# Kernel optimization log

Hardware: AMD Instinct MI355X
Metric: run time of the kernel (lower is better)

Reference implementation:

```python
import jax, jax.numpy as jnp
import numpy as np

L, B, T, TC, T1, D, DK, FF = 4, 4, 1024, 1024, 2048, 384, 256, 1536
TT = 0.1   # lamed blending coefficient (tt in (0,1] path)
EPS = 1e-5


def _ln(x, g, b):
    m = jnp.mean(x, axis=-1, keepdims=True)
    v = jnp.mean((x - m) ** 2, axis=-1, keepdims=True)
    return (x - m) * jax.lax.rsqrt(v + EPS) * g + b


def setup_inputs() -> dict:
    key = jax.random.key(0)
    ks = jax.random.split(key, 16)
    s = 0.02
    return {
        "tgt": jax.random.normal(ks[0], (B, T, D), jnp.float32),
        "memory": jax.random.normal(ks[1], (B, T1, DK), jnp.float32),
        "score_c": jax.random.normal(ks[2], (L, B, TC, T1), jnp.float32),
        "out_c": jax.random.normal(ks[3], (L, B, TC, D), jnp.float32),
        "Wq": jax.random.normal(ks[4], (L, D, D), jnp.float32) * s,
        "bq": jnp.zeros((L, D), jnp.float32),
        "Wk": jax.random.normal(ks[5], (L, D, DK), jnp.float32) * s,
        "bk": jnp.zeros((L, D), jnp.float32),
        "Wv": jax.random.normal(ks[6], (L, D, DK), jnp.float32) * s,
        "bv": jnp.zeros((L, D), jnp.float32),
        "Wkn": jax.random.normal(ks[7], (L, D, D), jnp.float32) * s,
        "bkn": jnp.zeros((L, D), jnp.float32),
        "Wun": jax.random.normal(ks[8], (L, D, D), jnp.float32) * s,
        "bun": jnp.zeros((L, D), jnp.float32),
        "W1": jax.random.normal(ks[9], (L, FF, D), jnp.float32) * s,
        "b1": jnp.zeros((L, FF), jnp.float32),
        "W2": jax.random.normal(ks[10], (L, D, FF), jnp.float32) * s,
        "b2": jnp.zeros((L, D), jnp.float32),
        "g1": jnp.ones((L, D), jnp.float32),
        "be1": jnp.zeros((L, D), jnp.float32),
        "g2": jnp.ones((L, D), jnp.float32),
        "be2": jnp.zeros((L, D), jnp.float32),
    }


def reference(tgt, memory, score_c, out_c, Wq, bq, Wk, bk, Wv, bv,
              Wkn, bkn, Wun, bun, W1, b1, W2, b2, g1, be1, g2, be2):
    scale = 1.0 / np.sqrt(D)
    x = tgt
    for l in range(L):  # fixed small layer count
        # cross-attention q/k/v (n_head = 1)
        q = jnp.einsum('btd,ed->bte', x, Wq[l]) + bq[l]            # [B,T,D]
        k = jnp.einsum('bsk,ek->bse', memory, Wk[l]) + bk[l]       # [B,T1,D]
        v = jnp.einsum('bsk,ek->bse', memory, Wv[l]) + bv[l]       # [B,T1,D]
        att = jnp.einsum('bte,bse->bts', q, k) * scale             # [B,T,T1]
        # blended score path (tt in (0,1])
        unk = jnp.einsum('btd,ed->bte', x, Wun[l]) + bun[l]        # [B,T,D]
        kno = jnp.einsum('bcd,ed->bce', out_c[l], Wkn[l]) + bkn[l] # [B,TC,D]
        score1 = jnp.einsum('bte,bce->btc', unk, kno) * scale      # [B,T,TC]
        mixed = jnp.einsum('btc,bcs->bts', score1, score_c[l])     # [B,T,T1]
        blended = TT * jax.nn.softmax(mixed, axis=-1) \
                  + (1.0 - TT) * jax.nn.softmax(att, axis=-1)
        z = jnp.einsum('bts,bse->bte', blended, v)                 # [B,T,D]
        x = _ln(x + z, g1[l], be1[l])
        h = jax.nn.relu(jnp.einsum('btd,fd->btf', x, W1[l]) + b1[l])
        y2 = jnp.einsum('btf,df->btd', h, W2[l]) + b2[l]
        x = _ln(x + y2, g2[l], be2[l])
    return x
```

## Files before the change

### kernel.cpp

```cpp
#include <hip/hip_runtime.h>
#include <math.h>

#define Lc 4
#define Bc 4
#define Tc 1024
#define TCc 1024
#define T1c 2048
#define Dc 384
#define DKc 256
#define FFc 1536
#define TTc 0.1f
#define EPSc 1e-5f

typedef unsigned short u16;
typedef __attribute__((ext_vector_type(8))) __bf16 bf16x8;
typedef __attribute__((ext_vector_type(8))) _Float16 f16x8;
typedef __attribute__((ext_vector_type(4))) float f32x4;

__device__ inline u16 f2bf(float f) {
  union { float f; unsigned u; } x; x.f = f;
  unsigned r = x.u + 0x7fffu + ((x.u >> 16) & 1u);
  return (u16)(r >> 16);
}

struct CDesc { const float* src; u16* dst; long n4; };
struct CPack { CDesc d[16]; long tot4; int nd; };

__global__ void cvt_multi(CPack P) {
  long i = (long)blockIdx.x * 256 + threadIdx.x;
  const long st = (long)gridDim.x * 256;
  for (; i < P.tot4; i += st) {
    long r = i; int g = 0;
    while (g < P.nd - 1 && r >= P.d[g].n4) { r -= P.d[g].n4; ++g; }
    float4 v = ((const float4*)P.d[g].src)[r];
    ushort4 o;
    o.x = f2bf(v.x); o.y = f2bf(v.y); o.z = f2bf(v.z); o.w = f2bf(v.w);
    ((ushort4*)P.d[g].dst)[r] = o;
  }
}

__global__ void concat_bias(const float* __restrict__ a, const float* __restrict__ b,
                            float* __restrict__ o) {
  int l = blockIdx.x, t = threadIdx.x;
  o[l * 768 + t] = (t < Dc) ? a[l * Dc + t] : b[l * Dc + t - Dc];
}

__global__ __launch_bounds__(256) void transpose_cvt(const float* __restrict__ src,
                                                     u16* __restrict__ dst) {
  __shared__ float t[64 * 65];
  const int z = blockIdx.z;
  const float* s = src + (long)z * TCc * T1c;
  u16* d = dst + (long)z * T1c * TCc;
  const int s0 = blockIdx.x * 64, c0 = blockIdx.y * 64;
  const int tc = threadIdx.x >> 4;
  const int tx = (threadIdx.x & 15) * 4;
#pragma unroll
  for (int it = 0; it < 4; ++it) {
    const int c = tc + it * 16;
    float4 v = *(const float4*)(s + (long)(c0 + c) * T1c + s0 + tx);
    float* q = t + c * 65 + tx;
    q[0] = v.x; q[1] = v.y; q[2] = v.z; q[3] = v.w;
  }
  __syncthreads();
#pragma unroll
  for (int it = 0; it < 4; ++it) {
    const int srow = tc + it * 16;
    u16 o[4];
#pragma unroll
    for (int k2 = 0; k2 < 4; ++k2) o[k2] = f2bf(t[(tx + k2) * 65 + srow]);
    *(ushort4*)(d + (long)(s0 + srow) * TCc + c0 + tx) = *(ushort4*)o;
  }
}

template<int BIAS_MODE, int RELU, int OUT_MODE, int SWIZ>
__global__ __launch_bounds__(256) void gemm_bt(
    const u16* __restrict__ A, const u16* __restrict__ B,
    void* __restrict__ C, const float* __restrict__ bias,
    float alpha, int N, int K, int lda, int ldb,
    long sA, long sB, long sC, long sBias, int ksplit, long sSlab, int bdivA)
{
  __shared__ __attribute__((aligned(16))) u16 As[128 * 32];
  __shared__ __attribute__((aligned(16))) u16 Bs[128 * 32];
  const int bz = blockIdx.z;
  const int b = bz / ksplit;
  const int kc = bz - b * ksplit;
  const int ba = b / bdivA;
  const int Klen = K / ksplit;
  const int k0 = kc * Klen;
  const u16* Ab = A + (long)ba * sA;
  const u16* Bb = B + (long)b * sB;
  long tm, tn;
  if (SWIZ) {
    const int id = blockIdx.y * 16 + blockIdx.x;
    tm = (long)(id >> 4) * 128;
    tn = (long)(2 * (id & 7) + ((id >> 3) & 1)) * 128;
  } else {
    tm = (long)blockIdx.y * 128; tn = (long)blockIdx.x * 128;
  }
  const int tid = threadIdx.x;
  const int lane = tid & 63, wv = tid >> 6;
  const int wm = (wv >> 1) * 64, wn = (wv & 1) * 64;
  const int q = lane >> 4, r = lane & 15;
  const int ldr = lane >> 2;
  const int ldc = (lane & 3) * 8;

  const u16* gA0 = Ab + (tm + wv * 32 + ldr) * (long)lda + k0 + ldc;
  const u16* gA1 = gA0 + 16 * (long)lda;
  const u16* gB0 = Bb + (tn + wv * 32 + ldr) * (long)ldb + k0 + ldc;
  const u16* gB1 = gB0 + 16 * (long)ldb;
  u16* dA0 = As + (wv * 32 + ldr) * 32 + ldc;
  u16* dA1 = dA0 + 16 * 32;
  u16* dB0 = Bs + (wv * 32 + ldr) * 32 + ldc;
  u16* dB1 = dB0 + 16 * 32;

  const f32x4 zero4 = {0.0f, 0.0f, 0.0f, 0.0f};
  f32x4 acc[4][4];
#pragma unroll
  for (int i = 0; i < 4; ++i)
#pragma unroll
    for (int j = 0; j < 4; ++j) acc[i][j] = zero4;

  uint4 ra0 = *(const uint4*)gA0;
  uint4 ra1 = *(const uint4*)gA1;
  uint4 rb0 = *(const uint4*)gB0;
  uint4 rb1 = *(const uint4*)gB1;

  const int iters = Klen >> 5;
  for (int it = 0; it < iters; ++it) {
    __builtin_amdgcn_s_barrier();
    *(uint4*)dA0 = ra0; *(uint4*)dA1 = ra1;
    *(uint4*)dB0 = rb0; *(uint4*)dB1 = rb1;
    __syncthreads();
    if (it + 1 < iters) {
      const long o = (long)(it + 1) * 32;
      ra0 = *(const uint4*)(gA0 + o);
      ra1 = *(const uint4*)(gA1 + o);
      rb0 = *(const uint4*)(gB0 + o);
      rb1 = *(const uint4*)(gB1 + o);
    }
    bf16x8 af[4], bfr[4];
#pragma unroll
    for (int i = 0; i < 4; ++i) {
      af[i]  = *(const bf16x8*)(As + (wm + i * 16 + r) * 32 + q * 8);
      bfr[i] = *(const bf16x8*)(Bs + (wn + i * 16 + r) * 32 + q * 8);
    }
#pragma unroll
    for (int i = 0; i < 4; ++i)
#pragma unroll
      for (int j = 0; j < 4; ++j)
        acc[i][j] = __builtin_amdgcn_mfma_f32_16x16x32_bf16(af[i], bfr[j], acc[i][j], 0, 0, 0);
  }

  const float* biasb = bias ? bias + (long)ba * sBias : nullptr;
#pragma unroll
  for (int i = 0; i < 4; ++i)
#pragma unroll
    for (int j = 0; j < 4; ++j)
#pragma unroll
      for (int v = 0; v < 4; ++v) {
        long row = tm + wm + i * 16 + q * 4 + v;
        long col = tn + wn + j * 16 + r;
        float val = acc[i][j][v] * alpha;
        if (BIAS_MODE == 1 && kc == 0) val += biasb[col];
        if (BIAS_MODE == 2 && kc == 0) val += biasb[row];
        if (RELU) val = fmaxf(val, 0.0f);
        long idx = (long)kc * sSlab + (long)b * sC + row * (long)N + col;
        if (OUT_MODE == 0)      ((float*)C)[idx] = val;
        else if (OUT_MODE == 1) ((u16*)C)[idx] = f2bf(val);
        else                    ((_Float16*)C)[idx] = (_Float16)val;
      }
}

__global__ __launch_bounds__(256) void blend_softmax(
    const _Float16* __restrict__ att, const _Float16* __restrict__ mixed,
    u16* __restrict__ out)
{
  const long row = blockIdx.x;
  const int tid = threadIdx.x;
  f16x8 av = *(const f16x8*)(att + row * T1c + tid * 8);
  f16x8 mv = *(const f16x8*)(mixed + row * T1c + tid * 8);
  float a[8], m[8];
#pragma unroll
  for (int i = 0; i < 8; ++i) { a[i] = (float)av[i]; m[i] = (float)mv[i]; }
  float amax = a[0], mmax = m[0];
#pragma unroll
  for (int i = 1; i < 8; ++i) { amax = fmaxf(amax, a[i]); mmax = fmaxf(mmax, m[i]); }
#pragma unroll
  for (int off = 32; off > 0; off >>= 1) {
    amax = fmaxf(amax, __shfl_xor(amax, off));
    mmax = fmaxf(mmax, __shfl_xor(mmax, off));
  }
  __shared__ float red[8];
  const int lane = tid & 63, wv = tid >> 6;
  if (lane == 0) { red[wv] = amax; red[4 + wv] = mmax; }
  __syncthreads();
  amax = fmaxf(fmaxf(red[0], red[1]), fmaxf(red[2], red[3]));
  mmax = fmaxf(fmaxf(red[4], red[5]), fmaxf(red[6], red[7]));
  __syncthreads();
  float asum = 0.f, msum = 0.f;
#pragma unroll
  for (int i = 0; i < 8; ++i) {
    a[i] = __expf(a[i] - amax); asum += a[i];
    m[i] = __expf(m[i] - mmax); msum += m[i];
  }
#pragma unroll
  for (int off = 32; off > 0; off >>= 1) {
    asum += __shfl_xor(asum, off);
    msum += __shfl_xor(msum, off);
  }
  if (lane == 0) { red[wv] = asum; red[4 + wv] = msum; }
  __syncthreads();
  asum = red[0] + red[1] + red[2] + red[3];
  msum = red[4] + red[5] + red[6] + red[7];
  const float ca = (1.0f - TTc) / asum, cm = TTc / msum;
  u16 o[8];
#pragma unroll
  for (int i = 0; i < 8; ++i) o[i] = f2bf(a[i] * ca + m[i] * cm);
  *(uint4*)(out + row * T1c + tid * 8) = *(uint4*)o;
}

__global__ __launch_bounds__(384) void add_ln4(
    const float* __restrict__ xin, const float* __restrict__ zs,
    const float* __restrict__ g, const float* __restrict__ be,
    float* __restrict__ xout, u16* __restrict__ xbf)
{
  const long row = blockIdx.x;
  const int d = threadIdx.x;
  const long SL = (long)Bc * Tc * Dc;
  const long o = row * Dc + d;
  float v = xin[o] + zs[o] + zs[SL + o] + zs[2 * SL + o] + zs[3 * SL + o];
  float s = v, s2 = v * v;
#pragma unroll
  for (int off = 32; off > 0; off >>= 1) {
    s  += __shfl_xor(s, off);
    s2 += __shfl_xor(s2, off);
  }
  __shared__ float red[12];
  const int lane = d & 63, wv = d >> 6;
  if (lane == 0) { red[wv] = s; red[6 + wv] = s2; }
  __syncthreads();
  float S = 0.f, S2 = 0.f;
#pragma unroll
  for (int w = 0; w < 6; ++w) { S += red[w]; S2 += red[6 + w]; }
  const float mean = S * (1.0f / Dc);
  const float var  = S2 * (1.0f / Dc) - mean * mean;
  const float rstd = rsqrtf(var + EPSc);
  const float y = (v - mean) * rstd * g[d] + be[d];
  xout[o] = y;
  xbf[o] = f2bf(y);
}

extern "C" void kernel_launch(void* const* d_in, const int* in_sizes, int n_in,
                              void* d_out, int out_size, void* d_ws, size_t ws_size,
                              hipStream_t stream)
{
  const float* tgt     = (const float*)d_in[0];
  const float* memory  = (const float*)d_in[1];
  const float* score_c = (const float*)d_in[2];
  const float* out_c   = (const float*)d_in[3];
  const float* Wq  = (const float*)d_in[4];  const float* bq  = (const float*)d_in[5];
  const float* Wk  = (const float*)d_in[6];  const float* bk  = (const float*)d_in[7];
  const float* Wv  = (const float*)d_in[8];  const float* bv  = (const float*)d_in[9];
  const float* Wkn = (const float*)d_in[10]; const float* bkn = (const float*)d_in[11];
  const float* Wun = (const float*)d_in[12]; const float* bun = (const float*)d_in[13];
  const float* W1  = (const float*)d_in[14]; const float* b1  = (const float*)d_in[15];
  const float* W2  = (const float*)d_in[16]; const float* b2  = (const float*)d_in[17];
  const float* g1  = (const float*)d_in[18]; const float* be1 = (const float*)d_in[19];
  const float* g2  = (const float*)d_in[20]; const float* be2 = (const float*)d_in[21];
  (void)in_sizes; (void)n_in; (void)out_size;

  char* p = (char*)d_ws;
  auto alloc = [&](size_t b) { char* r = p; p += (b + 255) & ~(size_t)255; return r; };

  u16* wk_bf   = (u16*)alloc((size_t)Lc * Dc * DKc * 2);
  u16* wv_bf   = (u16*)alloc((size_t)Lc * Dc * DKc * 2);
  u16* wkn_bf  = (u16*)alloc((size_t)Lc * Dc * Dc * 2);
  u16* w1_bf   = (u16*)alloc((size_t)Lc * FFc * Dc * 2);
  u16* w2_bf   = (u16*)alloc((size_t)Lc * Dc * FFc * 2);
  u16* wqu_bf  = (u16*)alloc((size_t)Lc * 2 * Dc * Dc * 2);
  float* bqu   = (float*)alloc((size_t)Lc * 2 * Dc * 4);
  u16* mem_bf  = (u16*)alloc((size_t)Bc * T1c * DKc * 2);
  u16* outc_bf = (u16*)alloc((size_t)Lc * Bc * TCc * Dc * 2);
  u16* x_bf    = (u16*)alloc((size_t)Bc * Tc * Dc * 2);
  float* xbuf  = (float*)alloc((size_t)Bc * Tc * Dc * 4);
  u16* qunk_bf = (u16*)alloc((size_t)Bc * Tc * 2 * Dc * 2);
  u16* k_all   = (u16*)alloc((size_t)Bc * T1c * Lc * Dc * 2);
  u16* vT_all  = (u16*)alloc((size_t)Bc * Lc * Dc * T1c * 2);
  u16* knoT_all = (u16*)alloc((size_t)Lc * Bc * Dc * TCc * 2);
  u16* M2T_all = (u16*)alloc((size_t)Lc * Bc * T1c * Dc * 2);
  u16* scT_all = (u16*)alloc((size_t)Lc * Bc * T1c * TCc * 2);
  _Float16* att   = (_Float16*)alloc((size_t)Bc * Tc * T1c * 2);
  _Float16* mixed = (_Float16*)alloc((size_t)Bc * Tc * T1c * 2);
  u16* blended = (u16*)alloc((size_t)Bc * Tc * T1c * 2);
  float* zslab = (float*)alloc((size_t)4 * Bc * Tc * Dc * 4);
  float* yslab = (float*)alloc((size_t)4 * Bc * Tc * Dc * 4);
  u16* h_bf    = (u16*)alloc((size_t)Bc * Tc * FFc * 2);

  if ((size_t)(p - (char*)d_ws) > ws_size) return;

  {
    CPack cp{}; int g = 0; long tot4 = 0;
    auto add = [&](const float* s, u16* d, long n) {
      cp.d[g].src = s; cp.d[g].dst = d; cp.d[g].n4 = n / 4; tot4 += n / 4; ++g;
    };
    add(Wk,  wk_bf,  (long)Lc * Dc * DKc);
    add(Wv,  wv_bf,  (long)Lc * Dc * DKc);
    add(Wkn, wkn_bf, (long)Lc * Dc * Dc);
    add(W1,  w1_bf,  (long)Lc * FFc * Dc);
    add(W2,  w2_bf,  (long)Lc * Dc * FFc);
    add(memory, mem_bf, (long)Bc * T1c * DKc);
    add(out_c, outc_bf, (long)Lc * Bc * TCc * Dc);
    add(tgt, x_bf, (long)Bc * Tc * Dc);
    for (int l = 0; l < Lc; ++l) {
      add(Wq + (long)l * Dc * Dc,  wqu_bf + (long)l * 2 * Dc * Dc, (long)Dc * Dc);
      add(Wun + (long)l * Dc * Dc, wqu_bf + (long)l * 2 * Dc * Dc + Dc * Dc, (long)Dc * Dc);
    }
    cp.nd = g; cp.tot4 = tot4;
    cvt_multi<<<4096, 256, 0, stream>>>(cp);
  }
  concat_bias<<<Lc, 2 * Dc, 0, stream>>>(bq, bun, bqu);

  transpose_cvt<<<dim3(T1c / 64, TCc / 64, Lc * Bc), 256, 0, stream>>>(score_c, scT_all);

  const float scale = 1.0f / sqrtf((float)Dc);
  const long SLAB = (long)Bc * Tc * Dc;

  gemm_bt<1,0,1,0><<<dim3(Lc*Dc/128, Bc*T1c/128, 1), 256, 0, stream>>>(
      mem_bf, wk_bf, k_all, bk, 1.0f, Lc*Dc, DKc, DKc, DKc, 0, 0, 0, 0, 1, 0, 1);
  gemm_bt<2,0,1,0><<<dim3(T1c/128, Lc*Dc/128, Bc), 256, 0, stream>>>(
      wv_bf, mem_bf, vT_all, bv, 1.0f, T1c, DKc, DKc, DKc,
      0, (long)T1c*DKc, (long)Lc*Dc*T1c, 0, 1, 0, 1);
  gemm_bt<2,0,1,0><<<dim3(TCc/128, Dc/128, Lc*Bc), 256, 0, stream>>>(
      wkn_bf, outc_bf, knoT_all, bkn, 1.0f, TCc, Dc, Dc, Dc,
      (long)Dc*Dc, (long)TCc*Dc, (long)Dc*TCc, Dc, 1, 0, Bc);
  gemm_bt<0,0,1,0><<<dim3(Dc/128, T1c/128, Lc*Bc), 256, 0, stream>>>(
      scT_all, knoT_all, M2T_all, nullptr, scale, Dc, TCc, TCc, TCc,
      (long)T1c*TCc, (long)Dc*TCc, (long)T1c*Dc, 0, 1, 0, 1);

  for (int l = 0; l < Lc; ++l) {
    gemm_bt<1,0,1,0><<<dim3(2*Dc/128, Bc*Tc/128, 1), 256, 0, stream>>>(
        x_bf, wqu_bf + (long)l*2*Dc*Dc, qunk_bf, bqu + l*2*Dc,
        1.0f, 2*Dc, Dc, Dc, Dc, 0, 0, 0, 0, 1, 0, 1);
    gemm_bt<0,0,2,0><<<dim3(T1c/128, Tc/128, Bc), 256, 0, stream>>>(
        qunk_bf, k_all + l*Dc, att, nullptr, scale, T1c, Dc, 2*Dc, Lc*Dc,
        (long)Tc*2*Dc, (long)T1c*Lc*Dc, (long)Tc*T1c, 0, 1, 0, 1);
    gemm_bt<0,0,2,1><<<dim3(T1c/128, Tc/128, Bc), 256, 0, stream>>>(
        qunk_bf + Dc, M2T_all + (long)l*Bc*T1c*Dc, mixed, nullptr, 1.0f,
        T1c, Dc, 2*Dc, Dc, (long)Tc*2*Dc, (long)T1c*Dc, (long)Tc*T1c, 0, 1, 0, 1);
    blend_softmax<<<Bc*Tc, 256, 0, stream>>>(att, mixed, blended);
    gemm_bt<0,0,0,0><<<dim3(Dc/128, Tc/128, Bc*4), 256, 0, stream>>>(
        blended, vT_all + (long)l*Dc*T1c, zslab, nullptr, 1.0f,
        Dc, T1c, T1c, T1c, (long)Tc*T1c, (long)Lc*Dc*T1c, (long)Tc*Dc, 0, 4, SLAB, 1);
    add_ln4<<<Bc*Tc, Dc, 0, stream>>>(
        (l == 0) ? tgt : xbuf, zslab, g1 + l*Dc, be1 + l*Dc, xbuf, x_bf);
    gemm_bt<1,1,1,0><<<dim3(FFc/128, Bc*Tc/128, 1), 256, 0, stream>>>(
        x_bf, w1_bf + (long)l*FFc*Dc, h_bf, b1 + l*FFc, 1.0f,
        FFc, Dc, Dc, Dc, 0, 0, 0, 0, 1, 0, 1);
    gemm_bt<1,0,0,0><<<dim3(Dc/128, Bc*Tc/128, 4), 256, 0, stream>>>(
        h_bf, w2_bf + (long)l*Dc*FFc, yslab, b2 + l*Dc, 1.0f,
        Dc, FFc, FFc, FFc, 0, 0, 0, 0, 4, SLAB, 1);
    add_ln4<<<Bc*Tc, Dc, 0, stream>>>(
        xbuf, yslab, g2 + l*Dc, be2 + l*Dc,
        (l == Lc - 1) ? (float*)d_out : xbuf, x_bf);
  }
}
```

Measured before the change: 975.1 us.

## Double-buffer GEMM LDS tiles and merge att/mixed GEMMs into one launch

The GEMM kernel now keeps two LDS buffers and alternates between them. This removes one of the two barriers per k-iteration, and the next global loads are issued before the sync. The att and mixed score GEMMs are fused into a single launch through a DUAL template mode that selects the B operand, output, A offset and alpha by blockIdx.z. This doubles the blocks per launch and cuts one kernel launch per layer. The att GEMM now also uses the swizzled tile order, and LDS use per block doubles, which may lower occupancy.

```diff
diff --git a/kernel.cpp b/kernel.cpp
--- a/kernel.cpp
+++ b/kernel.cpp
@@ -72,23 +72,30 @@
   }
 }
 
-template<int BIAS_MODE, int RELU, int OUT_MODE, int SWIZ>
+template<int BIAS_MODE, int RELU, int OUT_MODE, int SWIZ, int DUAL>
 __global__ __launch_bounds__(256) void gemm_bt(
     const u16* __restrict__ A, const u16* __restrict__ B,
     void* __restrict__ C, const float* __restrict__ bias,
     float alpha, int N, int K, int lda, int ldb,
-    long sA, long sB, long sC, long sBias, int ksplit, long sSlab, int bdivA)
+    long sA, long sB, long sC, long sBias, int ksplit, long sSlab, int bdivA,
+    const u16* __restrict__ B2, int ldb2, long sB2, int aoff2,
+    void* __restrict__ C2, float alpha2, int nbat)
 {
-  __shared__ __attribute__((aligned(16))) u16 As[128 * 32];
-  __shared__ __attribute__((aligned(16))) u16 Bs[128 * 32];
+  __shared__ __attribute__((aligned(16))) u16 As[2][128 * 32];
+  __shared__ __attribute__((aligned(16))) u16 Bs[2][128 * 32];
   const int bz = blockIdx.z;
-  const int b = bz / ksplit;
+  int b = bz / ksplit;
   const int kc = bz - b * ksplit;
+  const u16* Bp = B; int ldbv = ldb; long sBv = sB; void* Cp = C;
+  int aoff = 0; float al = alpha;
+  if (DUAL && b >= nbat) {
+    b -= nbat; Bp = B2; ldbv = ldb2; sBv = sB2; Cp = C2; aoff = aoff2; al = alpha2;
+  }
   const int ba = b / bdivA;
   const int Klen = K / ksplit;
   const int k0 = kc * Klen;
-  const u16* Ab = A + (long)ba * sA;
-  const u16* Bb = B + (long)b * sB;
+  const u16* Ab = A + (long)ba * sA + aoff;
+  const u16* Bb = Bp + (long)b * sBv;
   long tm, tn;
   if (SWIZ) {
     const int id = blockIdx.y * 16 + blockIdx.x;
@@ -106,12 +113,9 @@
 
   const u16* gA0 = Ab + (tm + wv * 32 + ldr) * (long)lda + k0 + ldc;
   const u16* gA1 = gA0 + 16 * (long)lda;
-  const u16* gB0 = Bb + (tn + wv * 32 + ldr) * (long)ldb + k0 + ldc;
-  const u16* gB1 = gB0 + 16 * (long)ldb;
-  u16* dA0 = As + (wv * 32 + ldr) * 32 + ldc;
-  u16* dA1 = dA0 + 16 * 32;
-  u16* dB0 = Bs + (wv * 32 + ldr) * 32 + ldc;
-  u16* dB1 = dB0 + 16 * 32;
+  const u16* gB0 = Bb + (tn + wv * 32 + ldr) * (long)ldbv + k0 + ldc;
+  const u16* gB1 = gB0 + 16 * (long)ldbv;
+  const int dof = (wv * 32 + ldr) * 32 + ldc;
 
   const f32x4 zero4 = {0.0f, 0.0f, 0.0f, 0.0f};
   f32x4 acc[4][4];
@@ -126,11 +130,12 @@
   uint4 rb1 = *(const uint4*)gB1;
 
   const int iters = Klen >> 5;
+  int cur = 0;
   for (int it = 0; it < iters; ++it) {
-    __builtin_amdgcn_s_barrier();
-    *(uint4*)dA0 = ra0; *(uint4*)dA1 = ra1;
-    *(uint4*)dB0 = rb0; *(uint4*)dB1 = rb1;
-    __syncthreads();
+    u16* a0 = As[cur] + dof;
+    u16* b0 = Bs[cur] + dof;
+    *(uint4*)a0 = ra0; *(uint4*)(a0 + 512) = ra1;
+    *(uint4*)b0 = rb0; *(uint4*)(b0 + 512) = rb1;
     if (it + 1 < iters) {
       const long o = (long)(it + 1) * 32;
       ra0 = *(const uint4*)(gA0 + o);
@@ -138,17 +143,19 @@
       rb0 = *(const uint4*)(gB0 + o);
       rb1 = *(const uint4*)(gB1 + o);
     }
+    __syncthreads();
     bf16x8 af[4], bfr[4];
 #pragma unroll
     for (int i = 0; i < 4; ++i) {
-      af[i]  = *(const bf16x8*)(As + (wm + i * 16 + r) * 32 + q * 8);
-      bfr[i] = *(const bf16x8*)(Bs + (wn + i * 16 + r) * 32 + q * 8);
+      af[i]  = *(const bf16x8*)(As[cur] + (wm + i * 16 + r) * 32 + q * 8);
+      bfr[i] = *(const bf16x8*)(Bs[cur] + (wn + i * 16 + r) * 32 + q * 8);
     }
 #pragma unroll
     for (int i = 0; i < 4; ++i)
 #pragma unroll
       for (int j = 0; j < 4; ++j)
         acc[i][j] = __builtin_amdgcn_mfma_f32_16x16x32_bf16(af[i], bfr[j], acc[i][j], 0, 0, 0);
+    cur ^= 1;
   }
 
   const float* biasb = bias ? bias + (long)ba * sBias : nullptr;
@@ -160,14 +167,14 @@
       for (int v = 0; v < 4; ++v) {
         long row = tm + wm + i * 16 + q * 4 + v;
         long col = tn + wn + j * 16 + r;
-        float val = acc[i][j][v] * alpha;
+        float val = acc[i][j][v] * al;
         if (BIAS_MODE == 1 && kc == 0) val += biasb[col];
         if (BIAS_MODE == 2 && kc == 0) val += biasb[row];
         if (RELU) val = fmaxf(val, 0.0f);
         long idx = (long)kc * sSlab + (long)b * sC + row * (long)N + col;
-        if (OUT_MODE == 0)      ((float*)C)[idx] = val;
-        else if (OUT_MODE == 1) ((u16*)C)[idx] = f2bf(val);
-        else                    ((_Float16*)C)[idx] = (_Float16)val;
+        if (OUT_MODE == 0)      ((float*)Cp)[idx] = val;
+        else if (OUT_MODE == 1) ((u16*)Cp)[idx] = f2bf(val);
+        else                    ((_Float16*)Cp)[idx] = (_Float16)val;
       }
 }
 
@@ -325,40 +332,46 @@
   const float scale = 1.0f / sqrtf((float)Dc);
   const long SLAB = (long)Bc * Tc * Dc;
 
-  gemm_bt<1,0,1,0><<<dim3(Lc*Dc/128, Bc*T1c/128, 1), 256, 0, stream>>>(
-      mem_bf, wk_bf, k_all, bk, 1.0f, Lc*Dc, DKc, DKc, DKc, 0, 0, 0, 0, 1, 0, 1);
-  gemm_bt<2,0,1,0><<<dim3(T1c/128, Lc*Dc/128, Bc), 256, 0, stream>>>(
+  gemm_bt<1,0,1,0,0><<<dim3(Lc*Dc/128, Bc*T1c/128, 1), 256, 0, stream>>>(
+      mem_bf, wk_bf, k_all, bk, 1.0f, Lc*Dc, DKc, DKc, DKc, 0, 0, 0, 0, 1, 0, 1,
+      nullptr, 0, 0, 0, nullptr, 0.f, 0);
+  gemm_bt<2,0,1,0,0><<<dim3(T1c/128, Lc*Dc/128, Bc), 256, 0, stream>>>(
       wv_bf, mem_bf, vT_all, bv, 1.0f, T1c, DKc, DKc, DKc,
-      0, (long)T1c*DKc, (long)Lc*Dc*T1c, 0, 1, 0, 1);
-  gemm_bt<2,0,1,0><<<dim3(TCc/128, Dc/128, Lc*Bc), 256, 0, stream>>>(
+      0, (long)T1c*DKc, (long)Lc*Dc*T1c, 0, 1, 0, 1,
+      nullptr, 0, 0, 0, nullptr, 0.f, 0);
+  gemm_bt<2,0,1,0,0><<<dim3(TCc/128, Dc/128, Lc*Bc), 256, 0, stream>>>(
       wkn_bf, outc_bf, knoT_all, bkn, 1.0f, TCc, Dc, Dc, Dc,
-      (long)Dc*Dc, (long)TCc*Dc, (long)Dc*TCc, Dc, 1, 0, Bc);
-  gemm_bt<0,0,1,0><<<dim3(Dc/128, T1c/128, Lc*Bc), 256, 0, stream>>>(
+      (long)Dc*Dc, (long)TCc*Dc, (long)Dc*TCc, Dc, 1, 0, Bc,
+      nullptr, 0, 0, 0, nullptr, 0.f, 0);
+  gemm_bt<0,0,1,0,0><<<dim3(Dc/128, T1c/128, Lc*Bc), 256, 0, stream>>>(
       scT_all, knoT_all, M2T_all, nullptr, scale, Dc, TCc, TCc, TCc,
-      (long)T1c*TCc, (long)Dc*TCc, (long)T1c*Dc, 0, 1, 0, 1);
+      (long)T1c*TCc, (long)Dc*TCc, (long)T1c*Dc, 0, 1, 0, 1,
+      nullptr, 0, 0, 0, nullptr, 0.f, 0);
 
   for (int l = 0; l < Lc; ++l) {
-    gemm_bt<1,0,1,0><<<dim3(2*Dc/128, Bc*Tc/128, 1), 256, 0, stream>>>(
+    gemm_bt<1,0,1,0,0><<<dim3(2*Dc/128, Bc*Tc/128, 1), 256, 0, stream>>>(
         x_bf, wqu_bf + (long)l*2*Dc*Dc, qunk_bf, bqu + l*2*Dc,
-        1.0f, 2*Dc, Dc, Dc, Dc, 0, 0, 0, 0, 1, 0, 1);
-    gemm_bt<0,0,2,0><<<dim3(T1c/128, Tc/128, Bc), 256, 0, stream>>>(
+        1.0f, 2*Dc, Dc, Dc, Dc, 0, 0, 0, 0, 1, 0, 1,
+        nullptr, 0, 0, 0, nullptr, 0.f, 0);
+    gemm_bt<0,0,2,1,1><<<dim3(T1c/128, Tc/128, 2*Bc), 256, 0, stream>>>(
         qunk_bf, k_all + l*Dc, att, nullptr, scale, T1c, Dc, 2*Dc, Lc*Dc,
-        (long)Tc*2*Dc, (long)T1c*Lc*Dc, (long)Tc*T1c, 0, 1, 0, 1);
-    gemm_bt<0,0,2,1><<<dim3(T1c/128, Tc/128, Bc), 256, 0, stream>>>(
-        qunk_bf + Dc, M2T_all + (long)l*Bc*T1c*Dc, mixed, nullptr, 1.0f,
-        T1c, Dc, 2*Dc, Dc, (long)Tc*2*Dc, (long)T1c*Dc, (long)Tc*T1c, 0, 1, 0, 1);
+        (long)Tc*2*Dc, (long)T1c*Lc*Dc, (long)Tc*T1c, 0, 1, 0, 1,
+        M2T_all + (long)l*Bc*T1c*Dc, Dc, (long)T1c*Dc, Dc, mixed, 1.0f, Bc);
     blend_softmax<<<Bc*Tc, 256, 0, stream>>>(att, mixed, blended);
-    gemm_bt<0,0,0,0><<<dim3(Dc/128, Tc/128, Bc*4), 256, 0, stream>>>(
+    gemm_bt<0,0,0,0,0><<<dim3(Dc/128, Tc/128, Bc*4), 256, 0, stream>>>(
         blended, vT_all + (long)l*Dc*T1c, zslab, nullptr, 1.0f,
-        Dc, T1c, T1c, T1c, (long)Tc*T1c, (long)Lc*Dc*T1c, (long)Tc*Dc, 0, 4, SLAB, 1);
+        Dc, T1c, T1c, T1c, (long)Tc*T1c, (long)Lc*Dc*T1c, (long)Tc*Dc, 0, 4, SLAB, 1,
+        nullptr, 0, 0, 0, nullptr, 0.f, 0);
     add_ln4<<<Bc*Tc, Dc, 0, stream>>>(
         (l == 0) ? tgt : xbuf, zslab, g1 + l*Dc, be1 + l*Dc, xbuf, x_bf);
-    gemm_bt<1,1,1,0><<<dim3(FFc/128, Bc*Tc/128, 1), 256, 0, stream>>>(
+    gemm_bt<1,1,1,0,0><<<dim3(FFc/128, Bc*Tc/128, 1), 256, 0, stream>>>(
         x_bf, w1_bf + (long)l*FFc*Dc, h_bf, b1 + l*FFc, 1.0f,
-        FFc, Dc, Dc, Dc, 0, 0, 0, 0, 1, 0, 1);
-    gemm_bt<1,0,0,0><<<dim3(Dc/128, Bc*Tc/128, 4), 256, 0, stream>>>(
+        FFc, Dc, Dc, Dc, 0, 0, 0, 0, 1, 0, 1,
+        nullptr, 0, 0, 0, nullptr, 0.f, 0);
+    gemm_bt<1,0,0,0,0><<<dim3(Dc/128, Bc*Tc/128, 4), 256, 0, stream>>>(
         h_bf, w2_bf + (long)l*Dc*FFc, yslab, b2 + l*Dc, 1.0f,
-        Dc, FFc, FFc, FFc, 0, 0, 0, 0, 4, SLAB, 1);
+        Dc, FFc, FFc, FFc, 0, 0, 0, 0, 4, SLAB, 1,
+        nullptr, 0, 0, 0, nullptr, 0.f, 0);
     add_ln4<<<Bc*Tc, Dc, 0, stream>>>(
         xbuf, yslab, g2 + l*Dc, be2 + l*Dc,
         (l == Lc - 1) ? (float*)d_out : xbuf, x_bf);
```

Result: faster. 953.0 us (-2.3%).
